# Performance work log

Measured on AMD Instinct MI355X. Metric: run time of the kernel, lower is better.

Reference implementation:

```python
import jax, jax.numpy as jnp
import numpy as np

SCALE = 30.0
MARGIN = 0.5
COS_M = float(np.cos(MARGIN))
SIN_M = float(np.sin(MARGIN))
TH = float(np.cos(np.pi - MARGIN))
MM = float(np.sin(np.pi - MARGIN) * MARGIN)
LN_EPS = 1e-7

B, S, H = 16, 2048, 1024
N_SPANS = 64
N_CLASSES = 4096


def setup_inputs() -> dict:
    key = jax.random.key(0)
    k1, k2, k3, k4, k5 = jax.random.split(key, 5)
    encoder_layer = jax.random.normal(k1, (B, S, H), dtype=jnp.float32)
    ln_gamma = jnp.ones((H,), jnp.float32)
    ln_beta = jnp.zeros((H,), jnp.float32)
    # xavier-uniform-like init for arcface head weight [out, in]
    limit = float(np.sqrt(6.0 / (N_CLASSES + H)))
    arc_weight = jax.random.uniform(k2, (N_CLASSES, H), jnp.float32, -limit, limit)
    heads = jax.random.randint(k3, (B, N_SPANS), 0, S - 32).astype(jnp.int32)
    lens = jax.random.randint(k4, (B, N_SPANS), 1, 33).astype(jnp.int32)
    tails = heads + lens  # guaranteed head < tail <= S
    labels = jax.random.randint(k5, (B, N_SPANS), 0, N_CLASSES).astype(jnp.int32)
    return {
        "encoder_layer": encoder_layer,
        "ln_gamma": ln_gamma,
        "ln_beta": ln_beta,
        "arc_weight": arc_weight,
        "span_head_idxs": heads,
        "span_tail_idxs": tails,
        "labels": labels,
    }


def _span_mean(encoder_layer, heads, tails):
    # fused ragged segment-mean via inclusive prefix sums over the seq dim
    # csum: [B, S+1, H], csum[b, t] = sum of encoder_layer[b, :t]
    csum = jnp.concatenate(
        [jnp.zeros_like(encoder_layer[:, :1]), jnp.cumsum(encoder_layer, axis=1)], axis=1
    )
    gather = lambda idx: jnp.take_along_axis(csum, idx[:, :, None].astype(jnp.int32), axis=1)
    sums = gather(tails) - gather(heads)  # [B, n_spans, H]
    counts = (tails - heads).astype(encoder_layer.dtype)[:, :, None]
    return sums / counts


def _layer_norm(x, gamma, beta):
    mu = jnp.mean(x, axis=-1, keepdims=True)
    var = jnp.mean(jnp.square(x - mu), axis=-1, keepdims=True)
    return (x - mu) * jax.lax.rsqrt(var + LN_EPS) * gamma + beta


def _l2norm(x):
    return x / jnp.maximum(jnp.linalg.norm(x, axis=-1, keepdims=True), 1e-12)


def reference(encoder_layer, ln_gamma, ln_beta, arc_weight, span_head_idxs, span_tail_idxs, labels):
    emb = _span_mean(encoder_layer, span_head_idxs, span_tail_idxs)  # [B, n_spans, H]
    emb = _layer_norm(emb, ln_gamma, ln_beta)
    emb = emb.reshape(-1, emb.shape[-1])  # [B*n_spans, H]
    lab = labels.reshape(-1)
    # ArcMarginProduct: cosine similarity
    cosine = (_l2norm(emb) @ _l2norm(arc_weight).T).astype(jnp.float32)  # [N, C]
    sine = jnp.sqrt(jnp.clip(1.0 - jnp.square(cosine), 0.0))
    phi = cosine * COS_M - sine * SIN_M
    phi = jnp.where(cosine > TH, phi, cosine - MM)
    onehot = jax.nn.one_hot(lab, cosine.shape[-1], dtype=cosine.dtype)
    logits = (onehot * phi + (1.0 - onehot) * cosine) * SCALE
    # mean cross entropy (all labels valid, ignore_index unused)
    logp = jax.nn.log_softmax(logits, axis=-1)
    nll = -jnp.take_along_axis(logp, lab[:, None].astype(jnp.int32), axis=1)[:, 0]
    return jnp.mean(nll)
```

## Files before the change

kernel.cpp:

```cpp
#include <hip/hip_runtime.h>
#include <hip/hip_bf16.h>
#include <math.h>

#define B_     16
#define S_     2048
#define H_     1024
#define NS_    64
#define NC_    4096
#define NROWS  1024

#define SCALE_ 30.0f
#define COS_M_ 0.8775825618903728f
#define SIN_M_ 0.479425538604203f
#define TH_    (-0.8775825618903728f)
#define MM_    0.2397127693021015f
#define LN_EPS_ 1e-7f


__device__ __forceinline__ unsigned short f2bf(float f) {
    union { float f; unsigned int u; } v; v.f = f;
    unsigned int r = v.u + 0x7fffu + ((v.u >> 16) & 1u);
    return (unsigned short)(r >> 16);
}

__device__ __forceinline__ float block_sum(float v) {
    __shared__ float sb[4];
    #pragma unroll
    for (int off = 32; off > 0; off >>= 1) v += __shfl_down(v, off, 64);
    if ((threadIdx.x & 63) == 0) sb[threadIdx.x >> 6] = v;
    __syncthreads();
    float r = sb[0] + sb[1] + sb[2] + sb[3];
    __syncthreads();
    return r;
}

__device__ __forceinline__ float block_max(float v) {
    __shared__ float sb[4];
    #pragma unroll
    for (int off = 32; off > 0; off >>= 1) v = fmaxf(v, __shfl_down(v, off, 64));
    if ((threadIdx.x & 63) == 0) sb[threadIdx.x >> 6] = v;
    __syncthreads();
    float r = fmaxf(fmaxf(sb[0], sb[1]), fmaxf(sb[2], sb[3]));
    __syncthreads();
    return r;
}

__device__ __forceinline__ void gload16(const void* g, void* l) {
    __builtin_amdgcn_global_load_lds(
        (const __attribute__((address_space(1))) unsigned int*)g,
        (__attribute__((address_space(3))) unsigned int*)l,
        16, 0, 0);
}

typedef short bf16x8 __attribute__((ext_vector_type(8)));
typedef float f32x4  __attribute__((ext_vector_type(4)));

__global__ __launch_bounds__(256) void span_kernel(
    const float* __restrict__ enc,
    const float* __restrict__ gamma,
    const float* __restrict__ beta,
    const int*   __restrict__ heads,
    const int*   __restrict__ tails,
    unsigned short* __restrict__ embn)
{
    const int span = blockIdx.x;
    const int b    = span >> 6;
    const int head = heads[span];
    const int tail = tails[span];
    const int cnt  = tail - head;
    const int tid  = threadIdx.x;

    const float4* base = (const float4*)(enc + ((size_t)b * S_ + head) * H_);
    float4 a; a.x = 0.f; a.y = 0.f; a.z = 0.f; a.w = 0.f;
    for (int s = 0; s < cnt; ++s) {
        float4 x = base[s * (H_ / 4) + tid];
        a.x += x.x; a.y += x.y; a.z += x.z; a.w += x.w;
    }
    const float inv = 1.0f / (float)cnt;
    float v0 = a.x * inv, v1 = a.y * inv, v2 = a.z * inv, v3 = a.w * inv;

    float mu = block_sum(v0 + v1 + v2 + v3) * (1.0f / H_);
    float d0 = v0 - mu, d1 = v1 - mu, d2 = v2 - mu, d3 = v3 - mu;
    float var = block_sum(d0*d0 + d1*d1 + d2*d2 + d3*d3) * (1.0f / H_);
    float rstd = rsqrtf(var + LN_EPS_);

    const int h = tid * 4;
    float y0 = d0 * rstd * gamma[h+0] + beta[h+0];
    float y1 = d1 * rstd * gamma[h+1] + beta[h+1];
    float y2 = d2 * rstd * gamma[h+2] + beta[h+2];
    float y3 = d3 * rstd * gamma[h+3] + beta[h+3];

    float ss = block_sum(y0*y0 + y1*y1 + y2*y2 + y3*y3);
    float invn = 1.0f / fmaxf(sqrtf(ss), 1e-12f);

    ushort4 o;
    o.x = f2bf(y0 * invn); o.y = f2bf(y1 * invn);
    o.z = f2bf(y2 * invn); o.w = f2bf(y3 * invn);
    *(ushort4*)(embn + (size_t)span * H_ + h) = o;
}

__global__ __launch_bounds__(256) void wnorm_kernel(
    const float* __restrict__ W,
    unsigned short* __restrict__ Wn)
{
    const int row = blockIdx.x;
    const int tid = threadIdx.x;
    float4 x = ((const float4*)(W + (size_t)row * H_))[tid];
    float ss = block_sum(x.x*x.x + x.y*x.y + x.z*x.z + x.w*x.w);
    float invn = 1.0f / fmaxf(sqrtf(ss), 1e-12f);
    ushort4 o;
    o.x = f2bf(x.x * invn); o.y = f2bf(x.y * invn);
    o.z = f2bf(x.z * invn); o.w = f2bf(x.w * invn);
    *(ushort4*)(Wn + (size_t)row * H_ + tid * 4) = o;
}

__global__ __launch_bounds__(256, 1) void gemm_kernel(
    const unsigned short* __restrict__ A,
    const unsigned short* __restrict__ Bw,
    float* __restrict__ C)
{
    __shared__ short As[128 * 32];
    __shared__ short Bs[128 * 32];

    const int m0   = blockIdx.x * 128;
    const int n0   = blockIdx.y * 128;
    const int tid  = threadIdx.x;
    const int lane = tid & 63;
    const int w    = tid >> 6;
    const int wm   = (w & 1) * 64;
    const int wn   = (w >> 1) * 64;
    const int lrow = lane & 15;
    const int q    = lane >> 4;

    const int rowA   = tid >> 2;
    const int kchunk = (tid & 3) * 8;

    f32x4 acc[4][4];
    #pragma unroll
    for (int i = 0; i < 4; ++i)
        #pragma unroll
        for (int j = 0; j < 4; ++j)
            acc[i][j] = (f32x4){0.f, 0.f, 0.f, 0.f};

    for (int k0 = 0; k0 < 1024; k0 += 32) {
        __syncthreads();
        #pragma unroll
        for (int t = 0; t < 2; ++t) {
            const int r = t * 64 + rowA;
            gload16(A  + ((size_t)(m0 + r) * 1024 + k0 + kchunk), &As[r * 32 + kchunk]);
            gload16(Bw + ((size_t)(n0 + r) * 1024 + k0 + kchunk), &Bs[r * 32 + kchunk]);
        }
        __syncthreads();

        bf16x8 af[4], bfr[4];
        #pragma unroll
        for (int i = 0; i < 4; ++i)
            af[i] = *(const bf16x8*)(&As[(wm + i * 16 + lrow) * 32 + q * 8]);
        #pragma unroll
        for (int j = 0; j < 4; ++j)
            bfr[j] = *(const bf16x8*)(&Bs[(wn + j * 16 + lrow) * 32 + q * 8]);

        #pragma unroll
        for (int i = 0; i < 4; ++i)
            #pragma unroll
            for (int j = 0; j < 4; ++j)
                acc[i][j] = __builtin_amdgcn_mfma_f32_16x16x32_bf16(af[i], bfr[j], acc[i][j], 0, 0, 0);
    }

    #pragma unroll
    for (int i = 0; i < 4; ++i) {
        const int rbase = m0 + wm + i * 16 + q * 4;
        #pragma unroll
        for (int j = 0; j < 4; ++j) {
            const int col = n0 + wn + j * 16 + lrow;
            #pragma unroll
            for (int r2 = 0; r2 < 4; ++r2)
                C[(size_t)(rbase + r2) * NC_ + col] = acc[i][j][r2];
        }
    }
}

__global__ __launch_bounds__(256) void ce_kernel(
    const float* __restrict__ cosine,
    const int*   __restrict__ labels,
    float* __restrict__ nll)
{
    __shared__ float s_lab;
    const int row = blockIdx.x;
    const int lab = labels[row];
    const int tid = threadIdx.x;
    const float4* c4 = (const float4*)(cosine + (size_t)row * NC_);

    float vals[16];
    float m = -1e30f;
    #pragma unroll
    for (int t = 0; t < 4; ++t) {
        float4 x = c4[tid + t * 256];
        const int cbase = (tid + t * 256) * 4;
        float xs[4] = {x.x, x.y, x.z, x.w};
        #pragma unroll
        for (int k = 0; k < 4; ++k) {
            float c = xs[k];
            float logit = c;
            if (cbase + k == lab) {
                float sine = sqrtf(fmaxf(1.0f - c * c, 0.0f));
                float phi  = c * COS_M_ - sine * SIN_M_;
                logit = (c > TH_) ? phi : (c - MM_);
            }
            logit *= SCALE_;
            vals[t * 4 + k] = logit;
            if (cbase + k == lab) s_lab = logit;
            m = fmaxf(m, logit);
        }
    }
    float gm = block_max(m);
    float e = 0.f;
    #pragma unroll
    for (int t = 0; t < 16; ++t) e += expf(vals[t] - gm);
    float se = block_sum(e);
    if (tid == 0) nll[row] = logf(se) + gm - s_lab;
}

__global__ __launch_bounds__(256) void mean_kernel(
    const float* __restrict__ nll, float* __restrict__ out)
{
    const int tid = threadIdx.x;
    float s = 0.f;
    #pragma unroll
    for (int t = 0; t < 4; ++t) s += nll[tid + t * 256];
    float tot = block_sum(s);
    if (tid == 0) out[0] = tot * (1.0f / NROWS);
}

extern "C" void kernel_launch(void* const* d_in, const int* in_sizes, int n_in,
                              void* d_out, int out_size, void* d_ws, size_t ws_size,
                              hipStream_t stream) {
    const float* enc    = (const float*)d_in[0];
    const float* gamma  = (const float*)d_in[1];
    const float* beta   = (const float*)d_in[2];
    const float* W      = (const float*)d_in[3];
    const int*   heads  = (const int*)d_in[4];
    const int*   tails  = (const int*)d_in[5];
    const int*   labels = (const int*)d_in[6];
    float* out = (float*)d_out;

    char* ws = (char*)d_ws;
    unsigned short* embn   = (unsigned short*)(ws);
    unsigned short* Wn     = (unsigned short*)(ws + (2u  << 20));
    float*          cosine = (float*)        (ws + (10u << 20));
    float*          nllbuf = (float*)        (ws + (26u << 20));

    span_kernel <<<NROWS, 256, 0, stream>>>(enc, gamma, beta, heads, tails, embn);
    wnorm_kernel<<<NC_,   256, 0, stream>>>(W, Wn);
    dim3 g3(NROWS / 128, NC_ / 128);
    gemm_kernel <<<g3,    256, 0, stream>>>(embn, Wn, cosine);
    ce_kernel   <<<NROWS, 256, 0, stream>>>(cosine, labels, nllbuf);
    mean_kernel <<<1,     256, 0, stream>>>(nllbuf, out);
}
```

Before: 233.9 us.

## Fuse ArcFace margin and softmax partials into GEMM epilogue, merge prep kernels

The GEMM epilogue now applies the ArcFace margin and computes per-row, per-column-block partial max and sum-exp, so the 16 MB cosine matrix is never written or re-read. The span and weight-normalization kernels are merged into one launch, and the CE and mean kernels are replaced by a single finalize kernel that merges the 32 partials per row. The GEMM M tile is halved to 64 so the grid has more blocks. In exchange the epilogue does extra shuffles and exps, and the finalize step is a single small block.

```diff
diff --git a/kernel.cpp b/kernel.cpp
--- a/kernel.cpp
+++ b/kernel.cpp
@@ -34,17 +34,6 @@
     return r;
 }
 
-__device__ __forceinline__ float block_max(float v) {
-    __shared__ float sb[4];
-    #pragma unroll
-    for (int off = 32; off > 0; off >>= 1) v = fmaxf(v, __shfl_down(v, off, 64));
-    if ((threadIdx.x & 63) == 0) sb[threadIdx.x >> 6] = v;
-    __syncthreads();
-    float r = fmaxf(fmaxf(sb[0], sb[1]), fmaxf(sb[2], sb[3]));
-    __syncthreads();
-    return r;
-}
-
 __device__ __forceinline__ void gload16(const void* g, void* l) {
     __builtin_amdgcn_global_load_lds(
         (const __attribute__((address_space(1))) unsigned int*)g,
@@ -55,20 +44,33 @@
 typedef short bf16x8 __attribute__((ext_vector_type(8)));
 typedef float f32x4  __attribute__((ext_vector_type(4)));
 
-__global__ __launch_bounds__(256) void span_kernel(
+__global__ __launch_bounds__(256) void prep_kernel(
     const float* __restrict__ enc,
     const float* __restrict__ gamma,
     const float* __restrict__ beta,
+    const float* __restrict__ W,
     const int*   __restrict__ heads,
     const int*   __restrict__ tails,
-    unsigned short* __restrict__ embn)
+    unsigned short* __restrict__ embn,
+    unsigned short* __restrict__ Wn)
 {
+    const int tid = threadIdx.x;
+    if (blockIdx.x >= NROWS) {
+        const int row = blockIdx.x - NROWS;
+        float4 x = ((const float4*)(W + (size_t)row * H_))[tid];
+        float ss = block_sum(x.x*x.x + x.y*x.y + x.z*x.z + x.w*x.w);
+        float invn = 1.0f / fmaxf(sqrtf(ss), 1e-12f);
+        ushort4 o;
+        o.x = f2bf(x.x * invn); o.y = f2bf(x.y * invn);
+        o.z = f2bf(x.z * invn); o.w = f2bf(x.w * invn);
+        *(ushort4*)(Wn + (size_t)row * H_ + tid * 4) = o;
+        return;
+    }
     const int span = blockIdx.x;
     const int b    = span >> 6;
     const int head = heads[span];
     const int tail = tails[span];
     const int cnt  = tail - head;
-    const int tid  = threadIdx.x;
 
     const float4* base = (const float4*)(enc + ((size_t)b * S_ + head) * H_);
     float4 a; a.x = 0.f; a.y = 0.f; a.z = 0.f; a.w = 0.f;
@@ -99,35 +101,26 @@
     *(ushort4*)(embn + (size_t)span * H_ + h) = o;
 }
 
-__global__ __launch_bounds__(256) void wnorm_kernel(
-    const float* __restrict__ W,
-    unsigned short* __restrict__ Wn)
-{
-    const int row = blockIdx.x;
-    const int tid = threadIdx.x;
-    float4 x = ((const float4*)(W + (size_t)row * H_))[tid];
-    float ss = block_sum(x.x*x.x + x.y*x.y + x.z*x.z + x.w*x.w);
-    float invn = 1.0f / fmaxf(sqrtf(ss), 1e-12f);
-    ushort4 o;
-    o.x = f2bf(x.x * invn); o.y = f2bf(x.y * invn);
-    o.z = f2bf(x.z * invn); o.w = f2bf(x.w * invn);
-    *(ushort4*)(Wn + (size_t)row * H_ + tid * 4) = o;
-}
-
-__global__ __launch_bounds__(256, 1) void gemm_kernel(
+__global__ __launch_bounds__(256) void gemm_arc_kernel(
     const unsigned short* __restrict__ A,
     const unsigned short* __restrict__ Bw,
-    float* __restrict__ C)
+    const int*   __restrict__ labels,
+    float* __restrict__ pmax,
+    float* __restrict__ psum,
+    float* __restrict__ labval)
 {
-    __shared__ short As[128 * 32];
+    __shared__ short As[64 * 32];
     __shared__ short Bs[128 * 32];
-
-    const int m0   = blockIdx.x * 128;
+    __shared__ float red_m[2][64];
+    __shared__ float red_s[2][64];
+
+    const int m0   = blockIdx.x * 64;
     const int n0   = blockIdx.y * 128;
+    const int nb   = blockIdx.y;
     const int tid  = threadIdx.x;
     const int lane = tid & 63;
     const int w    = tid >> 6;
-    const int wm   = (w & 1) * 64;
+    const int wm   = (w & 1) * 32;
     const int wn   = (w >> 1) * 64;
     const int lrow = lane & 15;
     const int q    = lane >> 4;
@@ -135,101 +128,115 @@
     const int rowA   = tid >> 2;
     const int kchunk = (tid & 3) * 8;
 
-    f32x4 acc[4][4];
-    #pragma unroll
-    for (int i = 0; i < 4; ++i)
+    f32x4 acc[2][4];
+    #pragma unroll
+    for (int i = 0; i < 2; ++i)
         #pragma unroll
         for (int j = 0; j < 4; ++j)
             acc[i][j] = (f32x4){0.f, 0.f, 0.f, 0.f};
 
     for (int k0 = 0; k0 < 1024; k0 += 32) {
         __syncthreads();
+        gload16(A + ((size_t)(m0 + rowA) * 1024 + k0 + kchunk), &As[rowA * 32 + kchunk]);
         #pragma unroll
         for (int t = 0; t < 2; ++t) {
             const int r = t * 64 + rowA;
-            gload16(A  + ((size_t)(m0 + r) * 1024 + k0 + kchunk), &As[r * 32 + kchunk]);
             gload16(Bw + ((size_t)(n0 + r) * 1024 + k0 + kchunk), &Bs[r * 32 + kchunk]);
         }
         __syncthreads();
 
-        bf16x8 af[4], bfr[4];
-        #pragma unroll
-        for (int i = 0; i < 4; ++i)
+        bf16x8 af[2], bfr[4];
+        #pragma unroll
+        for (int i = 0; i < 2; ++i)
             af[i] = *(const bf16x8*)(&As[(wm + i * 16 + lrow) * 32 + q * 8]);
         #pragma unroll
         for (int j = 0; j < 4; ++j)
             bfr[j] = *(const bf16x8*)(&Bs[(wn + j * 16 + lrow) * 32 + q * 8]);
 
         #pragma unroll
-        for (int i = 0; i < 4; ++i)
+        for (int i = 0; i < 2; ++i)
             #pragma unroll
             for (int j = 0; j < 4; ++j)
                 acc[i][j] = __builtin_amdgcn_mfma_f32_16x16x32_bf16(af[i], bfr[j], acc[i][j], 0, 0, 0);
     }
 
     #pragma unroll
-    for (int i = 0; i < 4; ++i) {
-        const int rbase = m0 + wm + i * 16 + q * 4;
-        #pragma unroll
-        for (int j = 0; j < 4; ++j) {
-            const int col = n0 + wn + j * 16 + lrow;
-            #pragma unroll
-            for (int r2 = 0; r2 < 4; ++r2)
-                C[(size_t)(rbase + r2) * NC_ + col] = acc[i][j][r2];
+    for (int i = 0; i < 2; ++i) {
+        #pragma unroll
+        for (int r2 = 0; r2 < 4; ++r2) {
+            const int rloc = wm + i * 16 + q * 4 + r2;
+            const int grow = m0 + rloc;
+            const int lab  = labels[grow];
+            float lg[4];
+            float lm = -1e30f;
+            #pragma unroll
+            for (int j = 0; j < 4; ++j) {
+                float c = acc[i][j][r2];
+                const int gcol = n0 + wn + j * 16 + lrow;
+                float logit = c * SCALE_;
+                if (gcol == lab) {
+                    float sine = sqrtf(fmaxf(1.0f - c * c, 0.0f));
+                    float phi  = c * COS_M_ - sine * SIN_M_;
+                    float pl   = (c > TH_) ? phi : (c - MM_);
+                    logit = pl * SCALE_;
+                    labval[grow] = logit;
+                }
+                lg[j] = logit;
+                lm = fmaxf(lm, logit);
+            }
+            float ls = 0.f;
+            #pragma unroll
+            for (int j = 0; j < 4; ++j) ls += expf(lg[j] - lm);
+            #pragma unroll
+            for (int d = 1; d < 16; d <<= 1) {
+                float om = __shfl_xor(lm, d, 64);
+                float os = __shfl_xor(ls, d, 64);
+                float nm = fmaxf(lm, om);
+                ls = ls * expf(lm - nm) + os * expf(om - nm);
+                lm = nm;
+            }
+            if (lrow == 0) { red_m[w >> 1][rloc] = lm; red_s[w >> 1][rloc] = ls; }
         }
     }
-}
-
-__global__ __launch_bounds__(256) void ce_kernel(
-    const float* __restrict__ cosine,
-    const int*   __restrict__ labels,
-    float* __restrict__ nll)
+    __syncthreads();
+    if (tid < 64) {
+        float ma = red_m[0][tid], sa = red_s[0][tid];
+        float mb = red_m[1][tid], sb = red_s[1][tid];
+        float M = fmaxf(ma, mb);
+        float S = sa * expf(ma - M) + sb * expf(mb - M);
+        pmax[(size_t)nb * NROWS + m0 + tid] = M;
+        psum[(size_t)nb * NROWS + m0 + tid] = S;
+    }
+}
+
+__global__ __launch_bounds__(1024) void finalize_kernel(
+    const float* __restrict__ pmax,
+    const float* __restrict__ psum,
+    const float* __restrict__ labval,
+    float* __restrict__ out)
 {
-    __shared__ float s_lab;
-    const int row = blockIdx.x;
-    const int lab = labels[row];
-    const int tid = threadIdx.x;
-    const float4* c4 = (const float4*)(cosine + (size_t)row * NC_);
-
-    float vals[16];
-    float m = -1e30f;
-    #pragma unroll
-    for (int t = 0; t < 4; ++t) {
-        float4 x = c4[tid + t * 256];
-        const int cbase = (tid + t * 256) * 4;
-        float xs[4] = {x.x, x.y, x.z, x.w};
-        #pragma unroll
-        for (int k = 0; k < 4; ++k) {
-            float c = xs[k];
-            float logit = c;
-            if (cbase + k == lab) {
-                float sine = sqrtf(fmaxf(1.0f - c * c, 0.0f));
-                float phi  = c * COS_M_ - sine * SIN_M_;
-                logit = (c > TH_) ? phi : (c - MM_);
-            }
-            logit *= SCALE_;
-            vals[t * 4 + k] = logit;
-            if (cbase + k == lab) s_lab = logit;
-            m = fmaxf(m, logit);
-        }
-    }
-    float gm = block_max(m);
-    float e = 0.f;
-    #pragma unroll
-    for (int t = 0; t < 16; ++t) e += expf(vals[t] - gm);
-    float se = block_sum(e);
-    if (tid == 0) nll[row] = logf(se) + gm - s_lab;
-}
-
-__global__ __launch_bounds__(256) void mean_kernel(
-    const float* __restrict__ nll, float* __restrict__ out)
-{
-    const int tid = threadIdx.x;
-    float s = 0.f;
-    #pragma unroll
-    for (int t = 0; t < 4; ++t) s += nll[tid + t * 256];
-    float tot = block_sum(s);
-    if (tid == 0) out[0] = tot * (1.0f / NROWS);
+    __shared__ float sb[16];
+    const int row = threadIdx.x;
+    float m = pmax[row], s = psum[row];
+    #pragma unroll 4
+    for (int nbk = 1; nbk < 32; ++nbk) {
+        float om = pmax[nbk * NROWS + row];
+        float os = psum[nbk * NROWS + row];
+        float nm = fmaxf(m, om);
+        s = s * expf(m - nm) + os * expf(om - nm);
+        m = nm;
+    }
+    float nll = logf(s) + m - labval[row];
+    #pragma unroll
+    for (int off = 32; off > 0; off >>= 1) nll += __shfl_down(nll, off, 64);
+    if ((row & 63) == 0) sb[row >> 6] = nll;
+    __syncthreads();
+    if (row < 64) {
+        float v = (row < 16) ? sb[row] : 0.f;
+        #pragma unroll
+        for (int off = 8; off > 0; off >>= 1) v += __shfl_down(v, off, 64);
+        if (row == 0) out[0] = v * (1.0f / NROWS);
+    }
 }
 
 extern "C" void kernel_launch(void* const* d_in, const int* in_sizes, int n_in,
@@ -247,13 +254,12 @@
     char* ws = (char*)d_ws;
     unsigned short* embn   = (unsigned short*)(ws);
     unsigned short* Wn     = (unsigned short*)(ws + (2u  << 20));
-    float*          cosine = (float*)        (ws + (10u << 20));
-    float*          nllbuf = (float*)        (ws + (26u << 20));
-
-    span_kernel <<<NROWS, 256, 0, stream>>>(enc, gamma, beta, heads, tails, embn);
-    wnorm_kernel<<<NC_,   256, 0, stream>>>(W, Wn);
-    dim3 g3(NROWS / 128, NC_ / 128);
-    gemm_kernel <<<g3,    256, 0, stream>>>(embn, Wn, cosine);
-    ce_kernel   <<<NROWS, 256, 0, stream>>>(cosine, labels, nllbuf);
-    mean_kernel <<<1,     256, 0, stream>>>(nllbuf, out);
-}
+    float*          pmax   = (float*)        (ws + (10u << 20));
+    float*          psum   = (float*)        (ws + (10u << 20) + (128u << 10));
+    float*          labval = (float*)        (ws + (10u << 20) + (256u << 10));
+
+    prep_kernel<<<NROWS + NC_, 256, 0, stream>>>(enc, gamma, beta, W, heads, tails, embn, Wn);
+    dim3 g2(NROWS / 64, NC_ / 128);
+    gemm_arc_kernel<<<g2, 256, 0, stream>>>(embn, Wn, labels, pmax, psum, labval);
+    finalize_kernel<<<1, 1024, 0, stream>>>(pmax, psum, labval, out);
+}
```

Result: no change. 236.3 us (+1.0%).
